# Kernel tuning notes

Measured on AMD Instinct MI355X. Metric: run time of the kernel, lower is better.

The kernel has to match this reference:

```python
import jax, jax.numpy as jnp
import numpy as np

N, E, H, L, B = 50000, 1250000, 64, 64, 500
BN_EPS = 1e-5


def _bn(x, g, b):
    # training-mode BatchNorm1d: per-feature batch mean / biased var
    m = jnp.mean(x, axis=0)
    v = jnp.mean((x - m) ** 2, axis=0)
    return (x - m) * jax.lax.rsqrt(v + BN_EPS) * g + b


def _gconv(h, edge_attr, src, dst):
    # message: softplus(x_j + edge_attr); aggr='add'; eps=0 -> + (1+0)*h
    msg = jax.nn.softplus(h[src] + edge_attr)          # [E,H]
    agg = jax.ops.segment_sum(msg, dst, num_segments=N)  # [N,H]
    return agg + h


def setup_inputs() -> dict:
    key = jax.random.key(0)
    ks = jax.random.split(key, 24)
    s = 0.05
    inp = {
        "x": jax.random.normal(ks[0], (E, 1), jnp.float32),
        "node_type": jax.random.randint(ks[1], (N,), 0, 100),
        "edge_type": jax.random.randint(ks[2], (E,), 0, 100),
        "edge_index": jax.random.randint(ks[3], (2, E), 0, N),
        "batch": jnp.sort(jax.random.randint(ks[4], (N,), 0, B)),
        "node_emb": jax.random.normal(ks[5], (100, H)) * s,
        "edge_emb": jax.random.normal(ks[6], (100, H)) * s,
        "w_d1": jax.random.normal(ks[7], (H, 1)) * s,
        "b_d1": jnp.zeros((H,)),
        "g_d1": jnp.ones((H,)), "be_d1": jnp.zeros((H,)),
        "w_d2": jax.random.normal(ks[8], (H, H)) * s,
        "b_d2": jnp.zeros((H,)),
        "g_d2": jnp.ones((H,)), "be_d2": jnp.zeros((H,)),
        "g_c1": jnp.ones((H,)), "be_c1": jnp.zeros((H,)),
        "g_c2": jnp.ones((H,)), "be_c2": jnp.zeros((H,)),
        "g_c3": jnp.ones((H,)), "be_c3": jnp.zeros((H,)),
        "w_o1": jax.random.normal(ks[9], (H, 2 * H)) * s,
        "b_o1": jnp.zeros((H,)),
        "g_o1": jnp.ones((H,)), "be_o1": jnp.zeros((H,)),
        "w_o2": jax.random.normal(ks[10], (H // 2, H)) * s,
        "b_o2": jnp.zeros((H // 2,)),
        "g_o2": jnp.ones((H // 2,)), "be_o2": jnp.zeros((H // 2,)),
        "w_o3": jax.random.normal(ks[11], (2 * L, H // 2)) * s,
        "b_o3": jnp.zeros((2 * L,)),
    }
    return inp


def reference(x, node_type, edge_type, edge_index, batch,
              node_emb, edge_emb,
              w_d1, b_d1, g_d1, be_d1,
              w_d2, b_d2, g_d2, be_d2,
              g_c1, be_c1, g_c2, be_c2, g_c3, be_c3,
              w_o1, b_o1, g_o1, be_o1,
              w_o2, b_o2, g_o2, be_o2,
              w_o3, b_o3):
    act = jax.nn.softplus
    src, dst = edge_index[0], edge_index[1]
    node_attr = node_emb[node_type]                    # [N,H]
    ea = edge_emb[edge_type]                           # [E,H]
    d = act(_bn(x @ w_d1.T + b_d1, g_d1, be_d1))       # [E,H]
    d = _bn(d @ w_d2.T + b_d2, g_d2, be_d2)
    ea = d * ea
    h = node_attr
    h = act(_bn(_gconv(h, ea, src, dst), g_c1, be_c1))
    h = act(_bn(_gconv(h, ea, src, dst), g_c2, be_c2))
    h = _bn(_gconv(h, ea, src, dst), g_c3, be_c3)
    h_global = jax.ops.segment_sum(h, batch, num_segments=B)  # [B,H]
    nf = jnp.concatenate([h, h_global[batch]], axis=-1)       # [N,2H]
    nf = act(_bn(nf @ w_o1.T + b_o1, g_o1, be_o1))
    nf = act(_bn(nf @ w_o2.T + b_o2, g_o2, be_o2))
    out = nf @ w_o3.T + b_o3                           # [N,2L]
    return out[:, :L], out[:, L:]
```

## Files before the change

kernel.cpp:

```cpp
#include <hip/hip_runtime.h>
#include <stdint.h>

#define NN 50000
#define EE 1250000
#define BB 500
#define BN_EPS 1e-5f
#define LOG2E 1.44269504f
#define LN2 0.69314718f

#define NBKT 391
#define NPBSH 7
#define NB1 256
#define BPB 4883

#define HBLK 88
#define HEPB ((EE + HBLK - 1) / HBLK)
#define FHSC 65536.f
#define FHIN (1.f / 65536.f)

#define NSL 16

#define NTB 8192
#define XLO (-12.0f)
#define XHI (12.0f)
#define XSC ((float)NTB / (XHI - XLO))
#define DXT ((XHI - XLO) / (float)NTB)
#define TPMAX 8191.999f

using u16 = unsigned short;
using u32 = unsigned int;

__device__ __forceinline__ u16 f2bf(float f) {
    u32 u = __float_as_uint(f);
    return (u16)((u + 0x7fffu + ((u >> 16) & 1u)) >> 16);
}
__device__ __forceinline__ u32 pk2(float a, float b) { return (u32)f2bf(a) | ((u32)f2bf(b) << 16); }
__device__ __forceinline__ float sp(float z) {
    float t = __builtin_amdgcn_exp2f(-fabsf(z) * LOG2E);
    float l = __builtin_amdgcn_logf(1.f + t) * LN2;
    return fmaxf(z, 0.f) + l;
}
__device__ __forceinline__ float rl(float v, int l) {
    return __uint_as_float(__builtin_amdgcn_readlane(__float_as_uint(v), l));
}

constexpr size_t OFF_ESD  = 0;
constexpr size_t OFF_ROWP = OFF_ESD + (size_t)EE * 16;
constexpr size_t OFF_HA   = (OFF_ROWP + (size_t)(NN + 1) * 4 + 255) & ~(size_t)255;
constexpr size_t OFF_HB   = OFF_HA + (size_t)NN * 64 * 4;
constexpr size_t OFF_ZB   = OFF_HB + (size_t)NN * 64 * 4;
constexpr size_t OFF_TMAT = OFF_ZB;
constexpr size_t OFF_TOT  = OFF_TMAT + (size_t)NB1 * NBKT * 4;
constexpr size_t OFF_BBASE= OFF_TOT + (size_t)NBKT * 4;
constexpr size_t OFF_YTAB = OFF_ZB + (size_t)NN * 32 * 4;
constexpr size_t OFF_PTAB = OFF_YTAB + (size_t)(NTB + 1) * 64 * 4;
constexpr size_t OFF_W2T  = OFF_PTAB + (size_t)NTB * 64 * 4;
constexpr size_t OFF_B2F  = OFF_W2T + 4096 * 4;
constexpr size_t OFF_W1T  = OFF_B2F + 256;
constexpr size_t OFF_W2O  = OFF_W1T + 8192 * 4;
constexpr size_t OFF_W3T  = OFF_W2O + 2048 * 4;
constexpr size_t OFF_BPTR = OFF_W3T + 4096 * 4;
constexpr size_t OFF_HG   = (OFF_BPTR + (BB + 1) * 4 + 255) & ~(size_t)255;
constexpr size_t OFF_XSTAT= OFF_HG + (size_t)BB * 64 * 4;
constexpr size_t OFF_STY  = OFF_XSTAT + 16;
constexpr size_t OFF_FST  = OFF_STY + 128 * 8;
constexpr size_t ZERO_END = OFF_FST + 5 * NSL * 128 * 4;
constexpr size_t ZERO_BYTES = ZERO_END - OFF_HG;
constexpr size_t OFF_HPART= (ZERO_END + 255) & ~(size_t)255;

__global__ void __launch_bounds__(256) k_prep0(
        const float* __restrict__ w2, const float* __restrict__ b2,
        const float* __restrict__ w1, const float* __restrict__ wo2, const float* __restrict__ w3,
        const float* __restrict__ x, const int* __restrict__ batch, const int* __restrict__ dstv,
        float* __restrict__ w2T, float* __restrict__ b2f,
        float* __restrict__ w1T, float* __restrict__ w2T2, float* __restrict__ w3T,
        double* __restrict__ xstat, int* __restrict__ bptr, int* __restrict__ T) {
    int bx = blockIdx.x, t = threadIdx.x;
    if (bx < 16) {
        int idx = bx * 256 + t;
        int hin = idx >> 6, ho = idx & 63;
        w2T[idx] = w2[ho * 64 + hin];
        if (idx < 64) b2f[idx] = b2[idx];
    } else if (bx < 72) {
        int idx = (bx - 16) * 256 + t;
        if (idx < 8192) {
            int j = idx >> 6, ho = idx & 63;
            w1T[idx] = w1[ho * 128 + j];
        } else if (idx < 8192 + 2048) {
            int q = idx - 8192;
            int j = q >> 5, ho = q & 31;
            w2T2[q] = wo2[ho * 64 + j];
        } else if (idx < 8192 + 2048 + 4096) {
            int q = idx - 8192 - 2048;
            int j = q >> 7, jo = q & 127;
            w3T[q] = w3[jo * 32 + j];
        }
    } else if (bx < 584) {
        __shared__ float ls[256], lq[256];
        float s = 0, q = 0;
        for (int i = (bx - 72) * 256 + t; i < EE; i += 512 * 256) {
            float v = x[i]; s += v; q += v * v;
        }
        ls[t] = s; lq[t] = q; __syncthreads();
        for (int off = 128; off > 0; off >>= 1) {
            if (t < off) { ls[t] += ls[t + off]; lq[t] += lq[t + off]; }
            __syncthreads();
        }
        if (t == 0) { atomicAdd(&xstat[0], (double)ls[0]); atomicAdd(&xstat[1], (double)lq[0]); }
    } else if (bx < 780) {
        int n = (bx - 584) * 256 + t;
        if (n >= NN) return;
        int b = batch[n];
        int pb = (n == 0) ? -1 : batch[n - 1];
        for (int k = pb + 1; k <= b; k++) bptr[k] = n;
        if (n == NN - 1) { for (int k = b + 1; k <= BB; k++) bptr[k] = NN; }
    } else {
        __shared__ int hh[NBKT];
        for (int i = t; i < NBKT; i += 256) hh[i] = 0;
        __syncthreads();
        int bb = bx - 780;
        int e0 = bb * BPB;
        int e1 = e0 + BPB; if (e1 > EE) e1 = EE;
        for (int e = e0 + t; e < e1; e += 256)
            atomicAdd(&hh[dstv[e] >> NPBSH], 1);
        __syncthreads();
        for (int i = t; i < NBKT; i += 256)
            T[(size_t)bb * NBKT + i] = hh[i];
    }
}

__global__ void k_bscanA(int* __restrict__ T, int* __restrict__ tot) {
    __shared__ int ls[256];
    int b = blockIdx.x, t = threadIdx.x;
    int v = T[(size_t)t * NBKT + b];
    ls[t] = v; __syncthreads();
    for (int off = 1; off < 256; off <<= 1) {
        int a = ls[t]; int add = (t >= off) ? ls[t - off] : 0; __syncthreads();
        ls[t] = a + add; __syncthreads();
    }
    T[(size_t)t * NBKT + b] = ls[t] - v;
    if (t == 255) tot[b] = ls[255];
}

__global__ void __launch_bounds__(1024) k_binhist(
        const float* __restrict__ x, const int* __restrict__ src,
        const int* __restrict__ dstv, const int* __restrict__ etv,
        const int* __restrict__ T, const int* __restrict__ tot,
        int* __restrict__ bbase_g, int4* __restrict__ esd_tmp, int* __restrict__ hpart) {
    __shared__ int shb[3 * (NTB / 2)];
    int t = threadIdx.x;
    if (blockIdx.x < NB1) {
        int* cur = shb;
        int* sls = shb + 512;
        int v = 0;
        if (t < 512) { v = (t < NBKT) ? tot[t] : 0; sls[t] = v; }
        __syncthreads();
        for (int off = 1; off < 512; off <<= 1) {
            int a = 0;
            if (t < 512) { a = sls[t]; if (t >= off) a += sls[t - off]; }
            __syncthreads();
            if (t < 512) sls[t] = a;
            __syncthreads();
        }
        if (t < NBKT) {
            int base = sls[t] - v;
            cur[t] = base + T[(size_t)blockIdx.x * NBKT + t];
            if (blockIdx.x == 0) bbase_g[t] = base;
        }
        if (blockIdx.x == 0 && t == 0) bbase_g[NBKT] = EE;
        __syncthreads();
        int e0 = blockIdx.x * BPB;
        int e1 = e0 + BPB; if (e1 > EE) e1 = EE;
        for (int e = e0 + t; e < e1; e += 1024) {
            int d = dstv[e];
            int p = atomicAdd(&cur[d >> NPBSH], 1);
            float tp = fminf(fmaxf((x[e] - XLO) * XSC, 0.f), TPMAX);
            int i = (int)tp; float f = tp - (float)i;
            int4 vv; vv.x = src[e]; vv.y = etv[e] | ((d & 127) << 7); vv.z = i; vv.w = __float_as_int(f);
            esd_tmp[p] = vv;
        }
    } else {
        int* cnt = shb; int* sf = shb + NTB / 2; int* sf2 = shb + NTB;
        int bb = blockIdx.x - NB1;
        int e0 = bb * HEPB;
        int e1 = e0 + HEPB; if (e1 > EE) e1 = EE;
        int* outp = hpart + (size_t)bb * 3 * NTB;
        for (int half = 0; half < 2; half++) {
            for (int i = t; i < NTB / 2; i += 1024) { cnt[i] = 0; sf[i] = 0; sf2[i] = 0; }
            __syncthreads();
            int lo = half * (NTB / 2);
            for (int e = e0 + t; e < e1; e += 1024) {
                float tp = fminf(fmaxf((x[e] - XLO) * XSC, 0.f), TPMAX);
                int i = (int)tp;
                int li = i - lo;
                if ((unsigned)li < (unsigned)(NTB / 2)) {
                    float f = tp - (float)i;
                    atomicAdd(&cnt[li], 1);
                    atomicAdd(&sf[li], (int)(f * FHSC));
                    atomicAdd(&sf2[li], (int)(f * f * FHSC));
                }
            }
            __syncthreads();
            for (int i = t; i < NTB / 2; i += 1024) {
                outp[lo + i] = cnt[i];
                outp[NTB + lo + i] = sf[i];
                outp[2 * NTB + lo + i] = sf2[i];
            }
            __syncthreads();
        }
    }
}

__global__ void __launch_bounds__(256) k_locyt(
        const int4* __restrict__ esd_tmp, const int* __restrict__ bbase,
        int* __restrict__ row_ptr, int4* __restrict__ esd,
        const double* __restrict__ xstat, const float* __restrict__ w_d1,
        const float* __restrict__ g_d1, const float* __restrict__ be_d1,
        const float* __restrict__ w2T, const float* __restrict__ b2f,
        const int* __restrict__ hpart, float* __restrict__ ytab, double* __restrict__ sty) {
    __shared__ char shraw[65 * 64 * 4 + 192 * 4];
    int t = threadIdx.x;
    if (blockIdx.x < NBKT) {
        int* hist = (int*)shraw;
        int* ls   = hist + 128;
        int* cur  = ls + 128;
        int b = blockIdx.x;
        if (b == 0 && t == 0) row_ptr[NN] = EE;
        int base = bbase[b], end = bbase[b + 1];
        if (t < 128) hist[t] = 0;
        __syncthreads();
        for (int p = base + t; p < end; p += 256)
            atomicAdd(&hist[(esd_tmp[p].y >> 7) & 127], 1);
        __syncthreads();
        int v = 0;
        if (t < 128) { v = hist[t]; ls[t] = v; }
        __syncthreads();
        for (int off = 1; off < 128; off <<= 1) {
            int a = 0;
            if (t < 128) { a = ls[t]; if (t >= off) a += ls[t - off]; }
            __syncthreads();
            if (t < 128) ls[t] = a;
            __syncthreads();
        }
        if (t < 128) {
            int exc = ls[t] - v;
            cur[t] = base + exc;
            int n = (b << NPBSH) + t;
            if (n < NN) row_ptr[n] = base + exc;
        }
        __syncthreads();
        for (int p = base + t; p < end; p += 256) {
            int4 r = esd_tmp[p];
            int ld = (r.y >> 7) & 127;
            r.y &= 127;
            esd[atomicAdd(&cur[ld], 1)] = r;
        }
    } else {
        float (*kn)[64] = (float(*)[64])shraw;
        float* hs = (float*)(shraw + 65 * 64 * 4);
        int lane = t & 63, w = t >> 6;
        int g = blockIdx.x - NBKT;
        double inv = 1.0 / (double)EE;
        double mx = xstat[0] * inv;
        double vx = xstat[1] * inv - mx * mx; if (vx < 0) vx = 0;
        float wd = w_d1[lane];
        float Aw = wd * rsqrtf((float)vx * wd * wd + BN_EPS) * g_d1[lane];
        float Cw = be_d1[lane];
        for (int kk = w; kk < 65; kk += 4) {
            int idx = (g << 6) + kk;
            float xi = XLO + (float)idx * DXT;
            float tt = xi - (float)mx;
            float d1L = sp(fmaf(Aw, tt, Cw));
            float y = b2f[lane];
            #pragma unroll
            for (int hin = 0; hin < 64; hin++)
                y = fmaf(rl(d1L, hin), w2T[hin * 64 + lane], y);
            kn[kk][lane] = y;
            if (kk < 64 || g == 127) ytab[(idx << 6) | lane] = y;
        }
        if (t < 192) {
            int slot = t >> 6, ii = t & 63;
            float s = 0.f;
            size_t off = (size_t)slot * NTB + (g << 6) + ii;
            for (int b = 0; b < HBLK; b++)
                s += (float)hpart[(size_t)b * 3 * NTB + off];
            hs[t] = (slot == 0) ? s : s * FHIN;
        }
        __syncthreads();
        if (t >= 64) return;
        double S = 0.0, Q = 0.0;
        float aprev = kn[0][lane];
        for (int ii = 0; ii < 64; ii++) {
            float c = hs[ii], f1 = hs[64 + ii], f2 = hs[128 + ii];
            float b = kn[ii + 1][lane];
            float a = aprev; aprev = b;
            float d = b - a;
            S += (double)(fmaf(c, a, d * f1));
            Q += (double)(fmaf(c * a, a, fmaf(2.f * a * d, f1, d * d * f2)));
        }
        atomicAdd(&sty[lane], S);
        atomicAdd(&sty[64 + lane], Q);
    }
}

__global__ void k_ypack(const float* __restrict__ ytab, const double* __restrict__ sty,
                        const float* __restrict__ g2, const float* __restrict__ be2,
                        u32* __restrict__ ptab) {
    int tid = blockIdx.x * 256 + threadIdx.x;
    int f = tid & 63;
    double inv = 1.0 / (double)EE;
    double m = sty[f] * inv;
    double var = sty[64 + f] * inv - m * m; if (var < 0) var = 0;
    float rstd = rsqrtf((float)var + BN_EPS);
    float sc0 = rstd * g2[f];
    float sc = sc0 * LOG2E;
    float sh = (be2[f] - (float)m * sc0) * LOG2E;
    float a = fmaf(ytab[tid], sc, sh);
    float b = fmaf(ytab[tid + 64], sc, sh);
    ptab[tid] = pk2(a, b - a);
}

__device__ __forceinline__ float edge_term(int4 ed, int lane, const u32* __restrict__ ptab,
                                           const float* __restrict__ emb) {
    u32 pr = ptab[(ed.z << 6) | lane];
    float f = __int_as_float(ed.w);
    float a = __uint_as_float(pr << 16);
    float d = __uint_as_float(pr & 0xffff0000u);
    float y = fmaf(f, d, a);
    return y * emb[(ed.y << 6) | lane];
}
__device__ __forceinline__ void sp2(float hv, float av, float& accm, float& accl) {
    float z = fmaf(hv, LOG2E, av);
    float t = __builtin_amdgcn_exp2f(-fabsf(z));
    accm += fmaxf(z, 0.f);
    accl += __builtin_amdgcn_logf(1.f + t);
}

__global__ void __launch_bounds__(128) k_agg(
        const float* __restrict__ h, const int4* __restrict__ esd, const int* __restrict__ row_ptr,
        const u32* __restrict__ ptab, const float* __restrict__ emb, float* __restrict__ hpre,
        float* __restrict__ stat) {
    int lane = threadIdx.x & 63;
    int w = threadIdx.x >> 6;
    int n = __builtin_amdgcn_readfirstlane((int)((blockIdx.x << 1) | w));
    int p0 = row_ptr[n], p1 = row_ptr[n + 1];
    float accm = 0.f, accl = 0.f;
    int p = p0;
    for (; p + 4 <= p1; p += 4) {
        int4 e0 = esd[p], e1 = esd[p + 1], e2 = esd[p + 2], e3 = esd[p + 3];
        float h0 = h[(e0.x << 6) | lane];
        float h1 = h[(e1.x << 6) | lane];
        float h2 = h[(e2.x << 6) | lane];
        float h3 = h[(e3.x << 6) | lane];
        float a0 = edge_term(e0, lane, ptab, emb);
        float a1 = edge_term(e1, lane, ptab, emb);
        float a2 = edge_term(e2, lane, ptab, emb);
        float a3 = edge_term(e3, lane, ptab, emb);
        sp2(h0, a0, accm, accl);
        sp2(h1, a1, accm, accl);
        sp2(h2, a2, accm, accl);
        sp2(h3, a3, accm, accl);
    }
    for (; p < p1; ++p) {
        int4 e0 = esd[p];
        float h0 = h[(e0.x << 6) | lane];
        sp2(h0, edge_term(e0, lane, ptab, emb), accm, accl);
    }
    int o = (n << 6) | lane;
    float val = fmaf(accm + accl, LN2, h[o]);
    hpre[o] = val;
    __shared__ float lsS[2][64], lsQ[2][64];
    lsS[w][lane] = val; lsQ[w][lane] = val * val;
    __syncthreads();
    if (w == 0) {
        int sl = ((int)blockIdx.x & (NSL - 1)) << 7;
        atomicAdd(&stat[sl + lane], lsS[0][lane] + lsS[1][lane]);
        atomicAdd(&stat[sl + 64 + lane], lsQ[0][lane] + lsQ[1][lane]);
    }
}

__global__ void __launch_bounds__(128) k_agg0(
        const int* __restrict__ nt, const float* __restrict__ nemb, const int4* __restrict__ esd,
        const int* __restrict__ row_ptr, const u32* __restrict__ ptab,
        const float* __restrict__ emb, float* __restrict__ hpre, float* __restrict__ stat) {
    int lane = threadIdx.x & 63;
    int w = threadIdx.x >> 6;
    int n = __builtin_amdgcn_readfirstlane((int)((blockIdx.x << 1) | w));
    int p0 = row_ptr[n], p1 = row_ptr[n + 1];
    float accm = 0.f, accl = 0.f;
    int p = p0;
    for (; p + 4 <= p1; p += 4) {
        int4 e0 = esd[p], e1 = esd[p + 1], e2 = esd[p + 2], e3 = esd[p + 3];
        float h0 = nemb[(nt[e0.x] << 6) | lane];
        float h1 = nemb[(nt[e1.x] << 6) | lane];
        float h2 = nemb[(nt[e2.x] << 6) | lane];
        float h3 = nemb[(nt[e3.x] << 6) | lane];
        float a0 = edge_term(e0, lane, ptab, emb);
        float a1 = edge_term(e1, lane, ptab, emb);
        float a2 = edge_term(e2, lane, ptab, emb);
        float a3 = edge_term(e3, lane, ptab, emb);
        sp2(h0, a0, accm, accl);
        sp2(h1, a1, accm, accl);
        sp2(h2, a2, accm, accl);
        sp2(h3, a3, accm, accl);
    }
    for (; p < p1; ++p) {
        int4 e0 = esd[p];
        float h0 = nemb[(nt[e0.x] << 6) | lane];
        sp2(h0, edge_term(e0, lane, ptab, emb), accm, accl);
    }
    float val = fmaf(accm + accl, LN2, nemb[(nt[n] << 6) | lane]);
    hpre[(n << 6) | lane] = val;
    __shared__ float lsS[2][64], lsQ[2][64];
    lsS[w][lane] = val; lsQ[w][lane] = val * val;
    __syncthreads();
    if (w == 0) {
        int sl = ((int)blockIdx.x & (NSL - 1)) << 7;
        atomicAdd(&stat[sl + lane], lsS[0][lane] + lsS[1][lane]);
        atomicAdd(&stat[sl + 64 + lane], lsQ[0][lane] + lsQ[1][lane]);
    }
}

__global__ void __launch_bounds__(256) k_bn(
        const float* __restrict__ in, float* __restrict__ out,
        const float* __restrict__ stat, const float* __restrict__ g,
        const float* __restrict__ be, int rows, int logC, int act) {
    int C = 1 << logC;
    __shared__ float scl[64], shl[64];
    int t = threadIdx.x;
    if (t < C) {
        float s = 0.f, q = 0.f;
        #pragma unroll
        for (int sl = 0; sl < NSL; sl++) {
            s += stat[(sl << 7) + t];
            q += stat[(sl << 7) + 64 + t];
        }
        float inv = 1.f / (float)rows;
        float m = s * inv;
        float var = q * inv - m * m; if (var < 0.f) var = 0.f;
        float rstd = rsqrtf(var + BN_EPS);
        float sc = rstd * g[t];
        scl[t] = sc; shl[t] = be[t] - m * sc;
    }
    __syncthreads();
    size_t total = (size_t)rows << logC;
    size_t i = (size_t)blockIdx.x * 256 + t;
    if (i >= total) return;
    int f = (int)(i & (C - 1));
    float val = fmaf(in[i], scl[f], shl[f]);
    out[i] = act ? sp(val) : val;
}

__global__ void __launch_bounds__(256) k_hg2(
        const float* __restrict__ h, const int* __restrict__ bptr, float* __restrict__ hg) {
    int b = blockIdx.x;
    int lane = threadIdx.x & 63, w = threadIdx.x >> 6;
    int n0 = bptr[b], n1 = bptr[b + 1];
    float acc = 0.f;
    for (int n = n0 + w; n < n1; n += 4)
        acc += h[(n << 6) | lane];
    __shared__ float ls[256];
    ls[threadIdx.x] = acc; __syncthreads();
    if (threadIdx.x < 64)
        hg[(b << 6) | lane] = ls[lane] + ls[64 + lane] + ls[128 + lane] + ls[192 + lane];
}

#define O1NPW 4
__global__ void __launch_bounds__(256) k_o1(
        const float* __restrict__ h, const float* __restrict__ hg, const int* __restrict__ batch,
        const float* __restrict__ w1T, const float* __restrict__ b1, float* __restrict__ z1,
        float* __restrict__ stat) {
    int lane = threadIdx.x & 63;
    int wv = (blockIdx.x * 256 + (int)threadIdx.x) >> 6;
    int n0 = __builtin_amdgcn_readfirstlane(wv * O1NPW);
    float hl[O1NPW], gl[O1NPW], acc[O1NPW];
    float bl = b1[lane];
    #pragma unroll
    for (int k = 0; k < O1NPW; k++) {
        int n = n0 + k;
        hl[k] = h[(n << 6) | lane];
        gl[k] = hg[(batch[n] << 6) | lane];
        acc[k] = bl;
    }
    #pragma unroll
    for (int j = 0; j < 64; j++) {
        float w = w1T[(j << 6) | lane];
        #pragma unroll
        for (int k = 0; k < O1NPW; k++)
            acc[k] = fmaf(rl(hl[k], j), w, acc[k]);
    }
    #pragma unroll
    for (int j = 0; j < 64; j++) {
        float w = w1T[((64 + j) << 6) | lane];
        #pragma unroll
        for (int k = 0; k < O1NPW; k++)
            acc[k] = fmaf(rl(gl[k], j), w, acc[k]);
    }
    float s = 0.f, q = 0.f;
    #pragma unroll
    for (int k = 0; k < O1NPW; k++) {
        z1[((n0 + k) << 6) | lane] = acc[k];
        s += acc[k]; q += acc[k] * acc[k];
    }
    __shared__ float lsS[4][64], lsQ[4][64];
    int w = threadIdx.x >> 6;
    lsS[w][lane] = s; lsQ[w][lane] = q; __syncthreads();
    if (threadIdx.x < 128) {
        int f = threadIdx.x & 63; bool isq = threadIdx.x >= 64;
        float r = 0.f;
        #pragma unroll
        for (int j = 0; j < 4; j++) r += isq ? lsQ[j][f] : lsS[j][f];
        int sl = ((int)blockIdx.x & (NSL - 1)) << 7;
        atomicAdd(&stat[sl + (isq ? 64 : 0) + f], r);
    }
}

__global__ void __launch_bounds__(256) k_o2(
        const float* __restrict__ o1v, const float* __restrict__ w2T2,
        const float* __restrict__ b2, float* __restrict__ z2, float* __restrict__ stat) {
    int lane = threadIdx.x & 63;
    int ho = lane & 31;
    int wv = (blockIdx.x * 256 + (int)threadIdx.x) >> 6;
    int n0 = __builtin_amdgcn_readfirstlane(wv * 8);
    float xr[8], acc[4];
    #pragma unroll
    for (int k = 0; k < 8; k++) {
        int n = n0 + k; if (n >= NN) n = NN - 1;
        xr[k] = o1v[(n << 6) | lane];
    }
    float bl = b2[ho];
    #pragma unroll
    for (int k = 0; k < 4; k++) acc[k] = bl;
    #pragma unroll
    for (int j = 0; j < 64; j++) {
        float w = w2T2[(j << 5) | ho];
        #pragma unroll
        for (int k = 0; k < 4; k++) {
            float slo = rl(xr[k], j);
            float shi = rl(xr[4 + k], j);
            float v = (lane < 32) ? slo : shi;
            acc[k] = fmaf(v, w, acc[k]);
        }
    }
    int nbase = n0 + ((lane >> 5) << 2);
    float s = 0.f, q = 0.f;
    #pragma unroll
    for (int k = 0; k < 4; k++) {
        if (nbase + k < NN) {
            z2[((nbase + k) << 5) | ho] = acc[k];
            s += acc[k]; q += acc[k] * acc[k];
        }
    }
    __shared__ float lsS[4][64], lsQ[4][64];
    int w = threadIdx.x >> 6;
    lsS[w][lane] = s; lsQ[w][lane] = q; __syncthreads();
    if (threadIdx.x < 64) {
        int f = threadIdx.x & 31; bool isq = threadIdx.x >= 32;
        float r = 0.f;
        #pragma unroll
        for (int j = 0; j < 4; j++)
            r += isq ? (lsQ[j][f] + lsQ[j][32 + f]) : (lsS[j][f] + lsS[j][32 + f]);
        int sl = ((int)blockIdx.x & (NSL - 1)) << 7;
        atomicAdd(&stat[sl + (isq ? 64 : 0) + f], r);
    }
}

__global__ void __launch_bounds__(256) k_o3(
        const float* __restrict__ o2v, const float* __restrict__ w3T,
        const float* __restrict__ b3, float* __restrict__ outp) {
    int lane = threadIdx.x & 63;
    int wv = (blockIdx.x * 256 + (int)threadIdx.x) >> 6;
    int n0 = __builtin_amdgcn_readfirstlane((wv >> 1) << 2);
    int jo = (((wv & 1) << 6) + lane);
    if (n0 >= NN) return;
    float zl[4], acc[4];
    float bl = b3[jo];
    #pragma unroll
    for (int k = 0; k < 4; k++) {
        zl[k] = o2v[((n0 + k) << 5) | (lane & 31)];
        acc[k] = bl;
    }
    #pragma unroll
    for (int j = 0; j < 32; j++) {
        float w = w3T[(j << 7) | jo];
        #pragma unroll
        for (int k = 0; k < 4; k++)
            acc[k] = fmaf(rl(zl[k], j), w, acc[k]);
    }
    #pragma unroll
    for (int k = 0; k < 4; k++) {
        int n = n0 + k;
        size_t dsti = (jo < 64) ? ((size_t)(n << 6) + jo)
                                : ((size_t)NN * 64 + (size_t)(n << 6) + (jo - 64));
        outp[dsti] = acc[k];
    }
}

extern "C" void kernel_launch(void* const* d_in, const int* in_sizes, int n_in,
                              void* d_out, int out_size, void* d_ws, size_t ws_size,
                              hipStream_t stream) {
    const float* x        = (const float*)d_in[0];
    const int* node_type  = (const int*)d_in[1];
    const int* edge_type  = (const int*)d_in[2];
    const int* edge_index = (const int*)d_in[3];
    const int* batch      = (const int*)d_in[4];
    const float* node_emb = (const float*)d_in[5];
    const float* edge_emb = (const float*)d_in[6];
    const float* w_d1 = (const float*)d_in[7];  const float* b_d1 = (const float*)d_in[8];
    const float* g_d1 = (const float*)d_in[9];  const float* be_d1 = (const float*)d_in[10];
    const float* w_d2 = (const float*)d_in[11]; const float* b_d2 = (const float*)d_in[12];
    const float* g_d2 = (const float*)d_in[13]; const float* be_d2 = (const float*)d_in[14];
    const float* g_c1 = (const float*)d_in[15]; const float* be_c1 = (const float*)d_in[16];
    const float* g_c2 = (const float*)d_in[17]; const float* be_c2 = (const float*)d_in[18];
    const float* g_c3 = (const float*)d_in[19]; const float* be_c3 = (const float*)d_in[20];
    const float* w_o1 = (const float*)d_in[21]; const float* b_o1 = (const float*)d_in[22];
    const float* g_o1 = (const float*)d_in[23]; const float* be_o1 = (const float*)d_in[24];
    const float* w_o2 = (const float*)d_in[25]; const float* b_o2 = (const float*)d_in[26];
    const float* g_o2 = (const float*)d_in[27]; const float* be_o2 = (const float*)d_in[28];
    const float* w_o3 = (const float*)d_in[29]; const float* b_o3 = (const float*)d_in[30];
    (void)b_d1;
    const int* src  = edge_index;
    const int* dstv = edge_index + EE;

    char* ws = (char*)d_ws;
    int4*  esd     = (int4*)(ws + OFF_ESD);
    int*   row_ptr = (int*)(ws + OFF_ROWP);
    float* hA   = (float*)(ws + OFF_HA);
    float* hB   = (float*)(ws + OFF_HB);
    float* zb   = (float*)(ws + OFF_ZB);
    int4*  esd_tmp = (int4*)(ws + OFF_HA);
    int*   hpart = (int*)(ws + OFF_HPART);
    int*   T    = (int*)(ws + OFF_TMAT);
    int*   tot  = (int*)(ws + OFF_TOT);
    int*   bbase= (int*)(ws + OFF_BBASE);
    float* ytab = (float*)(ws + OFF_YTAB);
    u32*   ptab = (u32*)(ws + OFF_PTAB);
    float* w2T  = (float*)(ws + OFF_W2T);
    float* b2f  = (float*)(ws + OFF_B2F);
    float* w1T  = (float*)(ws + OFF_W1T);
    float* w2T2 = (float*)(ws + OFF_W2O);
    float* w3T  = (float*)(ws + OFF_W3T);
    int*   bptr = (int*)(ws + OFF_BPTR);
    float* hg     = (float*)(ws + OFF_HG);
    double* xstat = (double*)(ws + OFF_XSTAT);
    double* sty   = (double*)(ws + OFF_STY);
    float* fst    = (float*)(ws + OFF_FST);
    float* st0 = fst;               float* st1 = fst + NSL * 128;
    float* st2 = fst + 2 * NSL * 128;
    float* st3 = fst + 3 * NSL * 128;
    float* st4 = fst + 4 * NSL * 128;

    hipMemsetAsync(ws + OFF_HG, 0, ZERO_BYTES, stream);

    k_prep0<<<1036, 256, 0, stream>>>(w_d2, b_d2, w_o1, w_o2, w_o3, x, batch, dstv,
                                      w2T, b2f, w1T, w2T2, w3T, xstat, bptr, T);
    k_bscanA<<<NBKT, 256, 0, stream>>>(T, tot);
    k_binhist<<<NB1 + HBLK, 1024, 0, stream>>>(x, src, dstv, edge_type, T, tot,
                                               bbase, esd_tmp, hpart);
    k_locyt<<<NBKT + 128, 256, 0, stream>>>(esd_tmp, bbase, row_ptr, esd,
                                            xstat, w_d1, g_d1, be_d1, w2T, b2f,
                                            hpart, ytab, sty);
    k_ypack<<<NTB * 64 / 256, 256, 0, stream>>>(ytab, sty, g_d2, be_d2, ptab);
    k_agg0<<<25000, 128, 0, stream>>>(node_type, node_emb, esd, row_ptr, ptab, edge_emb, hB, st0);
    k_bn<<<12500, 256, 0, stream>>>(hB, hB, st0, g_c1, be_c1, NN, 6, 1);
    k_agg<<<25000, 128, 0, stream>>>(hB, esd, row_ptr, ptab, edge_emb, hA, st1);
    k_bn<<<12500, 256, 0, stream>>>(hA, hA, st1, g_c2, be_c2, NN, 6, 1);
    k_agg<<<25000, 128, 0, stream>>>(hA, esd, row_ptr, ptab, edge_emb, hB, st2);
    k_bn<<<12500, 256, 0, stream>>>(hB, hB, st2, g_c3, be_c3, NN, 6, 0);
    k_hg2<<<BB, 256, 0, stream>>>(hB, bptr, hg);
    k_o1<<<3125, 256, 0, stream>>>(hB, hg, batch, w1T, b_o1, hA, st3);
    k_bn<<<12500, 256, 0, stream>>>(hA, hA, st3, g_o1, be_o1, NN, 6, 1);
    k_o2<<<1563, 256, 0, stream>>>(hA, w2T2, b_o2, zb, st4);
    k_bn<<<6250, 256, 0, stream>>>(zb, zb, st4, g_o2, be_o2, NN, 5, 1);
    k_o3<<<6250, 256, 0, stream>>>(zb, w3T, b_o3, (float*)d_out);
    (void)in_sizes; (void)n_in; (void)out_size; (void)ws_size;
}
```

Measured before the change: 563.2 us.

## Move BN statistics out of aggregation kernels into separate reduction kernel

The per-block shared-memory reduction, __syncthreads and global atomics are removed from the three graph aggregation kernels, and a new k_fstats kernel launched after each one computes the per-feature sum and sum of squares. The aim is to free the latency-bound gather kernels from block barriers and heavy atomic contention (25000 blocks each issuing atomics). The cost is three extra launches and an extra full read of the 50000x64 activation buffer. The remaining stat atomics also switch to unsafeAtomicAdd so hardware float atomics can be used.

```diff
diff --git a/kernel.cpp b/kernel.cpp
--- a/kernel.cpp
+++ b/kernel.cpp
@@ -338,11 +338,9 @@
 
 __global__ void __launch_bounds__(128) k_agg(
         const float* __restrict__ h, const int4* __restrict__ esd, const int* __restrict__ row_ptr,
-        const u32* __restrict__ ptab, const float* __restrict__ emb, float* __restrict__ hpre,
-        float* __restrict__ stat) {
+        const u32* __restrict__ ptab, const float* __restrict__ emb, float* __restrict__ hpre) {
     int lane = threadIdx.x & 63;
-    int w = threadIdx.x >> 6;
-    int n = __builtin_amdgcn_readfirstlane((int)((blockIdx.x << 1) | w));
+    int n = __builtin_amdgcn_readfirstlane((int)((blockIdx.x << 1) | (threadIdx.x >> 6)));
     int p0 = row_ptr[n], p1 = row_ptr[n + 1];
     float accm = 0.f, accl = 0.f;
     int p = p0;
@@ -367,25 +365,15 @@
         sp2(h0, edge_term(e0, lane, ptab, emb), accm, accl);
     }
     int o = (n << 6) | lane;
-    float val = fmaf(accm + accl, LN2, h[o]);
-    hpre[o] = val;
-    __shared__ float lsS[2][64], lsQ[2][64];
-    lsS[w][lane] = val; lsQ[w][lane] = val * val;
-    __syncthreads();
-    if (w == 0) {
-        int sl = ((int)blockIdx.x & (NSL - 1)) << 7;
-        atomicAdd(&stat[sl + lane], lsS[0][lane] + lsS[1][lane]);
-        atomicAdd(&stat[sl + 64 + lane], lsQ[0][lane] + lsQ[1][lane]);
-    }
+    hpre[o] = fmaf(accm + accl, LN2, h[o]);
 }
 
 __global__ void __launch_bounds__(128) k_agg0(
         const int* __restrict__ nt, const float* __restrict__ nemb, const int4* __restrict__ esd,
         const int* __restrict__ row_ptr, const u32* __restrict__ ptab,
-        const float* __restrict__ emb, float* __restrict__ hpre, float* __restrict__ stat) {
+        const float* __restrict__ emb, float* __restrict__ hpre) {
     int lane = threadIdx.x & 63;
-    int w = threadIdx.x >> 6;
-    int n = __builtin_amdgcn_readfirstlane((int)((blockIdx.x << 1) | w));
+    int n = __builtin_amdgcn_readfirstlane((int)((blockIdx.x << 1) | (threadIdx.x >> 6)));
     int p0 = row_ptr[n], p1 = row_ptr[n + 1];
     float accm = 0.f, accl = 0.f;
     int p = p0;
@@ -409,15 +397,27 @@
         float h0 = nemb[(nt[e0.x] << 6) | lane];
         sp2(h0, edge_term(e0, lane, ptab, emb), accm, accl);
     }
-    float val = fmaf(accm + accl, LN2, nemb[(nt[n] << 6) | lane]);
-    hpre[(n << 6) | lane] = val;
-    __shared__ float lsS[2][64], lsQ[2][64];
-    lsS[w][lane] = val; lsQ[w][lane] = val * val;
-    __syncthreads();
-    if (w == 0) {
+    hpre[(n << 6) | lane] = fmaf(accm + accl, LN2, nemb[(nt[n] << 6) | lane]);
+}
+
+__global__ void __launch_bounds__(256) k_fstats(
+        const float* __restrict__ v, int rows, float* __restrict__ stat) {
+    int f = threadIdx.x & 63;
+    int r0 = threadIdx.x >> 6;
+    float s = 0.f, q = 0.f;
+    for (int r = blockIdx.x * 4 + r0; r < rows; r += gridDim.x * 4) {
+        float val = v[(size_t)r * 64 + f];
+        s += val; q += val * val;
+    }
+    __shared__ float lsS[4][64], lsQ[4][64];
+    lsS[r0][f] = s; lsQ[r0][f] = q; __syncthreads();
+    if (threadIdx.x < 128) {
+        int ff = threadIdx.x & 63; bool isq = threadIdx.x >= 64;
+        float r = 0.f;
+        #pragma unroll
+        for (int j = 0; j < 4; j++) r += isq ? lsQ[j][ff] : lsS[j][ff];
         int sl = ((int)blockIdx.x & (NSL - 1)) << 7;
-        atomicAdd(&stat[sl + lane], lsS[0][lane] + lsS[1][lane]);
-        atomicAdd(&stat[sl + 64 + lane], lsQ[0][lane] + lsQ[1][lane]);
+        unsafeAtomicAdd(&stat[sl + (isq ? 64 : 0) + ff], r);
     }
 }
 
@@ -511,7 +511,7 @@
         #pragma unroll
         for (int j = 0; j < 4; j++) r += isq ? lsQ[j][f] : lsS[j][f];
         int sl = ((int)blockIdx.x & (NSL - 1)) << 7;
-        atomicAdd(&stat[sl + (isq ? 64 : 0) + f], r);
+        unsafeAtomicAdd(&stat[sl + (isq ? 64 : 0) + f], r);
     }
 }
 
@@ -561,7 +561,7 @@
         for (int j = 0; j < 4; j++)
             r += isq ? (lsQ[j][f] + lsQ[j][32 + f]) : (lsS[j][f] + lsS[j][32 + f]);
         int sl = ((int)blockIdx.x & (NSL - 1)) << 7;
-        atomicAdd(&stat[sl + (isq ? 64 : 0) + f], r);
+        unsafeAtomicAdd(&stat[sl + (isq ? 64 : 0) + f], r);
     }
 }
 
@@ -661,11 +661,14 @@
                                             xstat, w_d1, g_d1, be_d1, w2T, b2f,
                                             hpart, ytab, sty);
     k_ypack<<<NTB * 64 / 256, 256, 0, stream>>>(ytab, sty, g_d2, be_d2, ptab);
-    k_agg0<<<25000, 128, 0, stream>>>(node_type, node_emb, esd, row_ptr, ptab, edge_emb, hB, st0);
+    k_agg0<<<25000, 128, 0, stream>>>(node_type, node_emb, esd, row_ptr, ptab, edge_emb, hB);
+    k_fstats<<<1024, 256, 0, stream>>>(hB, NN, st0);
     k_bn<<<12500, 256, 0, stream>>>(hB, hB, st0, g_c1, be_c1, NN, 6, 1);
-    k_agg<<<25000, 128, 0, stream>>>(hB, esd, row_ptr, ptab, edge_emb, hA, st1);
+    k_agg<<<25000, 128, 0, stream>>>(hB, esd, row_ptr, ptab, edge_emb, hA);
+    k_fstats<<<1024, 256, 0, stream>>>(hA, NN, st1);
     k_bn<<<12500, 256, 0, stream>>>(hA, hA, st1, g_c2, be_c2, NN, 6, 1);
-    k_agg<<<25000, 128, 0, stream>>>(hA, esd, row_ptr, ptab, edge_emb, hB, st2);
+    k_agg<<<25000, 128, 0, stream>>>(hA, esd, row_ptr, ptab, edge_emb, hB);
+    k_fstats<<<1024, 256, 0, stream>>>(hB, NN, st2);
     k_bn<<<12500, 256, 0, stream>>>(hB, hB, st2, g_c3, be_c3, NN, 6, 0);
     k_hg2<<<BB, 256, 0, stream>>>(hB, bptr, hg);
     k_o1<<<3125, 256, 0, stream>>>(hB, hg, batch, w1T, b_o1, hA, st3);
```

After: 508.4 us. 9.7% less time.
